# Kernel tuning notes

Hardware: AMD Instinct MI355X
Metric: run time of the kernel (lower is better)

## Reference

```python
import jax, jax.numpy as jnp
import numpy as np

NUM_CLASSES = 4
GAMMA = 2.0          # FocalLoss gamma
T_ALPHA, T_BETA = 0.3, 0.7
SMOOTH = 1e-5
W_DICE, W_CE, W_BOUND = 1.0, 1.0, 0.01
INF = 1e12


def _dt1d(f):
    # min-plus 1D squared distance transform along last axis (brute Felzenszwalb)
    n = f.shape[-1]
    i = jnp.arange(n, dtype=f.dtype)
    d2 = (i[:, None] - i[None, :]) ** 2          # [n, n]
    return jnp.min(f[..., None, :] + d2, axis=-1)


def _edt(seed):
    # Euclidean distance from every voxel to the nearest True voxel in `seed`
    f = jnp.where(seed, 0.0, INF).astype(jnp.float32)
    for ax in range(f.ndim):
        f = jnp.moveaxis(_dt1d(jnp.moveaxis(f, ax, -1)), -1, ax)
    return jnp.sqrt(f)


def _sdf(mask):
    # signed distance map, matching compute_edt_map (mask: bool [D,H,W])
    s = mask.sum()
    size = mask.size
    dist_out = _edt(mask)        # scipy distance(1-mask)
    dist_in = _edt(~mask)        # scipy distance(mask)
    sdf = dist_out - dist_in
    sdf = jnp.where(s == 0, 1.0, jnp.where(s == size, -1.0, sdf))
    return sdf


def setup_inputs() -> dict:
    key = jax.random.key(0)
    k1, k2 = jax.random.split(key)
    preds = jax.random.normal(k1, (4, NUM_CLASSES, 64, 64, 64), dtype=jnp.float32)
    targets = jax.random.randint(k2, (4, 64, 64, 64), 0, NUM_CLASSES).astype(jnp.int64)
    return {"preds": preds, "targets": targets}


def reference(preds, targets):
    B = preds.shape[0]
    sp_dims = (2, 3, 4)

    probs = jax.nn.softmax(preds, axis=1)                       # [B,C,D,H,W]
    onehot = (targets[:, None] == jnp.arange(NUM_CLASSES)[None, :, None, None, None]).astype(preds.dtype)

    # ---- Tversky ----
    TP = jnp.sum(probs * onehot, axis=sp_dims)
    FP = jnp.sum(probs * (1.0 - onehot), axis=sp_dims)
    FN = jnp.sum((1.0 - probs) * onehot, axis=sp_dims)
    tversky = (TP + SMOOTH) / (TP + T_ALPHA * FP + T_BETA * FN + SMOOTH)
    l_dice = 1.0 - tversky.mean()

    # ---- Focal ----
    logp = jax.nn.log_softmax(preds, axis=1)
    ce = -jnp.take_along_axis(logp, targets[:, None], axis=1)[:, 0]   # [B,D,H,W]
    pt = jnp.exp(-ce)
    l_main = jnp.mean((1.0 - pt) ** GAMMA * ce)

    # ---- Boundary ----
    masks = targets[:, None] == jnp.arange(1, NUM_CLASSES)[None, :, None, None, None]  # [B,3,D,H,W] bool
    flat = masks.reshape((-1,) + masks.shape[2:])
    sdfs = jax.lax.map(_sdf, flat).reshape(masks.shape)               # [B,3,D,H,W]
    nonempty = jnp.sum(masks, axis=sp_dims) > 0                       # [B,3]
    contrib = jnp.mean(sdfs * probs[:, 1:NUM_CLASSES], axis=sp_dims)  # [B,3]
    l_bound = jnp.sum(jnp.where(nonempty, contrib, 0.0)) / (B * (NUM_CLASSES - 1) + 1e-8)

    return W_DICE * l_dice + W_CE * l_main + W_BOUND * l_bound
```

## Files before the change

kernel.cpp:

```cpp
#include <hip/hip_runtime.h>
#include <math.h>

#define SPATIAL 262144
#define NVOX    1048576
#define NVOL    12
#define FAR_D2  50000
#define NPART   13

typedef unsigned short u16x2 __attribute__((ext_vector_type(2)));
union pku { unsigned int u; u16x2 v; };

__device__ __forceinline__ unsigned int pk_min(unsigned int a, unsigned int b) {
    pku x, y; x.u = a; y.u = b;
    x.v = __builtin_elementwise_min(x.v, y.v);
    return x.u;
}
__device__ __forceinline__ unsigned int pk_max(unsigned int a, unsigned int b) {
    pku x, y; x.u = a; y.u = b;
    x.v = __builtin_elementwise_max(x.v, y.v);
    return x.u;
}

__device__ __forceinline__ int row_d2i(unsigned long long m, int i) {
    if (m == 0ull) return FAR_D2;
    unsigned long long right = m >> i;
    unsigned long long left  = m << (63 - i);
    int dr = right ? __builtin_ctzll(right) : 1000;
    int dl = left  ? __builtin_clzll(left)  : 1000;
    int d = (dr < dl) ? dr : dl;
    return d * d;
}

#define MINPLUS_PK(LA, ACC, LANE, W)                                            \
    {                                                                           \
        const int base = (W) * 8;                                               \
        _Pragma("unroll")                                                       \
        for (int jj = 0; jj < 8; ++jj) {                                        \
            unsigned int wv = LA[(base + jj) * 64 + (LANE)];                    \
            _Pragma("unroll")                                                   \
            for (int k = 0; k < 8; ++k) {                                       \
                int d = k - jj;                                                 \
                unsigned int dd = (unsigned int)(d * d);                        \
                ACC[k] = pk_min(ACC[k], wv + (dd | (dd << 16)));                \
            }                                                                   \
        }                                                                       \
        const int el_max = base, er_max = 56 - base;                            \
        int t = 1;                                                              \
        while (true) {                                                          \
            unsigned int am = 0;                                                \
            _Pragma("unroll")                                                   \
            for (int k = 0; k < 8; ++k) am = pk_max(am, ACC[k]);                \
            _Pragma("unroll")                                                   \
            for (int off = 32; off > 0; off >>= 1)                              \
                am = pk_max(am, (unsigned int)__shfl_xor((int)am, off, 64));    \
            int amx = (int)(am & 0xFFFFu), amy = (int)(am >> 16);               \
            int mm = (amx > amy) ? amx : amy;                                   \
            int dmax = (int)sqrtf((float)mm) + 1;     \
            int Tl = (dmax < el_max) ? dmax : el_max;                           \
            int Tr = (dmax < er_max) ? dmax : er_max;                           \
            int T = (Tl > Tr) ? Tl : Tr;                                        \
            if (t > T) break;                                                   \
            int tend = (T < t + 7) ? T : (t + 7);                               \
            for (; t <= tend; ++t) {                                            \
                if (t <= Tl) {                                                  \
                    unsigned int wv = LA[(base - t) * 64 + (LANE)];             \
                    _Pragma("unroll")                                           \
                    for (int k = 0; k < 8; ++k) {                               \
                        int d = t + k;                                          \
                        unsigned int dd = (unsigned int)(d * d);                \
                        ACC[k] = pk_min(ACC[k], wv + (dd | (dd << 16)));        \
                    }                                                           \
                }                                                               \
                if (t <= Tr) {                                                  \
                    unsigned int wv = LA[(base + 7 + t) * 64 + (LANE)];         \
                    _Pragma("unroll")                                           \
                    for (int k = 0; k < 8; ++k) {                               \
                        int d = t + 7 - k;                                      \
                        unsigned int dd = (unsigned int)(d * d);                \
                        ACC[k] = pk_min(ACC[k], wv + (dd | (dd << 16)));        \
                    }                                                           \
                }                                                               \
            }                                                                   \
        }                                                                       \
    }

__global__ __launch_bounds__(512) void dtxy_kernel(
        const int* __restrict__ targets, unsigned int* __restrict__ dtp) {
    __shared__ unsigned int la[4096];
    int blk = blockIdx.x;
    int v = blk >> 6, z = blk & 63;
    int b = v / 3, cls = (v % 3) + 1;
    const int* tp = targets + b * SPATIAL + z * 4096;
    int t = threadIdx.x, lane = t & 63, w = t >> 6;

    #pragma unroll
    for (int k = 0; k < 8; ++k) {
        int y = w * 8 + k;
        int tv = tp[y * 64 + lane];
        unsigned long long m = __ballot(tv == cls);
        int do2 = row_d2i(m, lane);
        int di2 = row_d2i(~m, lane);
        la[y * 64 + lane] = (unsigned int)do2 | ((unsigned int)di2 << 16);
    }
    __syncthreads();

    unsigned int acc[8];
    #pragma unroll
    for (int k = 0; k < 8; ++k) acc[k] = 0xFFFFFFFFu;
    MINPLUS_PK(la, acc, lane, w)

    size_t vol = (size_t)v * SPATIAL;
    #pragma unroll
    for (int k = 0; k < 8; ++k) {
        int i = w * 8 + k;
        dtp[vol + (size_t)z * 4096 + (size_t)i * 64 + lane] = acc[k];
    }
}

__global__ __launch_bounds__(512) void dtz_fused_kernel(
        const unsigned int* __restrict__ dtp, const float* __restrict__ preds,
        const int* __restrict__ targets,
        float* __restrict__ bound, float* __restrict__ rpart) {
    __shared__ unsigned int la[4096];
    int blk = blockIdx.x;
    int v = blk >> 6, y = blk & 63;
    int b = v / 3, cls = (v % 3) + 1;
    size_t vol = (size_t)v * SPATIAL;
    int t = threadIdx.x, lane = t & 63, w = t >> 6;

    #pragma unroll
    for (int k = 0; k < 8; ++k) {
        int idx = k * 512 + t;
        int zz = idx >> 6, x = idx & 63;
        la[idx] = dtp[vol + (size_t)zz * 4096 + (size_t)y * 64 + x];
    }
    __syncthreads();

    unsigned int acc[8];
    #pragma unroll
    for (int k = 0; k < 8; ++k) acc[k] = 0xFFFFFFFFu;
    MINPLUS_PK(la, acc, lane, w)

    const bool doRed = (cls == 1);
    float loc[NPART];
    #pragma unroll
    for (int k = 0; k < NPART; ++k) loc[k] = 0.0f;

    float partial = 0.0f;
    const float* pbase = preds + (size_t)b * 4 * SPATIAL;
    const int* tbase = targets + b * SPATIAL;
    #pragma unroll
    for (int k = 0; k < 8; ++k) {
        int i = w * 8 + k;
        size_t sp = (size_t)i * 4096 + (size_t)y * 64 + lane;
        float dout = (float)(acc[k] & 0xFFFFu);
        float din  = (float)(acc[k] >> 16);
        float sv = sqrtf(dout) - sqrtf(din);
        float p0 = pbase[sp], p1 = pbase[SPATIAL + sp];
        float p2 = pbase[2 * SPATIAL + sp], p3 = pbase[3 * SPATIAL + sp];
        float m = fmaxf(fmaxf(p0, p1), fmaxf(p2, p3));
        float e0 = __expf(p0 - m), e1 = __expf(p1 - m);
        float e2 = __expf(p2 - m), e3 = __expf(p3 - m);
        float s = e0 + e1 + e2 + e3;
        float inv = __builtin_amdgcn_rcpf(s);
        float ec = (cls == 1) ? e1 : (cls == 2) ? e2 : e3;
        partial += sv * (ec * inv);
        if (doRed) {
            int tv = tbase[sp];
            float q0 = e0 * inv, q1 = e1 * inv, q2 = e2 * inv, q3 = e3 * inv;
            float pl = (tv == 0) ? p0 : (tv == 1) ? p1 : (tv == 2) ? p2 : p3;
            float ce = __logf(s) + (m - pl);
            float qt = (tv == 0) ? q0 : (tv == 1) ? q1 : (tv == 2) ? q2 : q3;
            float om = 1.0f - qt;
            loc[0] += q0; loc[1] += q1; loc[2] += q2; loc[3] += q3;
            if (tv == 0)      { loc[4] += q0; loc[8]  += 1.f; }
            else if (tv == 1) { loc[5] += q1; loc[9]  += 1.f; }
            else if (tv == 2) { loc[6] += q2; loc[10] += 1.f; }
            else              { loc[7] += q3; loc[11] += 1.f; }
            loc[12] += om * om * ce;
        }
    }

    #pragma unroll
    for (int off = 32; off > 0; off >>= 1)
        partial += __shfl_down(partial, off, 64);
    __shared__ float ws8[8];
    if (lane == 0) ws8[w] = partial;

    if (doRed) {
        __shared__ float sred[NPART][8];
        #pragma unroll
        for (int k = 0; k < NPART; ++k) {
            float vv = loc[k];
            #pragma unroll
            for (int off = 32; off > 0; off >>= 1)
                vv += __shfl_down(vv, off, 64);
            loc[k] = vv;
        }
        if (lane == 0) {
            #pragma unroll
            for (int k = 0; k < NPART; ++k) sred[k][w] = loc[k];
        }
        __syncthreads();
        if (t < NPART) {
            float tot = 0.0f;
            #pragma unroll
            for (int i = 0; i < 8; ++i) tot += sred[t][i];
            rpart[(b * NPART + t) * 64 + y] = tot;
        }
    } else {
        __syncthreads();
    }
    if (t == 0) {
        float tot = 0.0f;
        #pragma unroll
        for (int i = 0; i < 8; ++i) tot += ws8[i];
        bound[blk] = tot;
    }
}

__global__ __launch_bounds__(256) void final_kernel(
        const float* __restrict__ rpart, const float* __restrict__ bound,
        float* __restrict__ out) {
    __shared__ float rowsum[52];
    __shared__ float bsum[12];
    int tid = threadIdx.x, lane = tid & 63, w = tid >> 6;

    for (int r = w; r < 52; r += 4) {
        float v = rpart[r * 64 + lane];
        #pragma unroll
        for (int off = 32; off > 0; off >>= 1)
            v += __shfl_down(v, off, 64);
        if (lane == 0) rowsum[r] = v;
    }
    for (int r = w; r < 12; r += 4) {
        float v = bound[r * 64 + lane];
        #pragma unroll
        for (int off = 32; off > 0; off >>= 1)
            v += __shfl_down(v, off, 64);
        if (lane == 0) bsum[r] = v;
    }
    __syncthreads();
    if (tid != 0) return;

    float tsum = 0.0f;
    for (int b = 0; b < 4; ++b)
        for (int c = 0; c < 4; ++c) {
            float S  = rowsum[b * NPART + c];
            float TP = rowsum[b * NPART + 4 + c];
            float CN = rowsum[b * NPART + 8 + c];
            float FP = S - TP;
            float FN = CN - TP;
            tsum += (TP + 1e-5f) / (TP + 0.3f * FP + 0.7f * FN + 1e-5f);
        }
    float l_dice = 1.0f - tsum / 16.0f;
    float l_main = (rowsum[12] + rowsum[NPART + 12] +
                    rowsum[2 * NPART + 12] + rowsum[3 * NPART + 12]) / (float)NVOX;
    float bs = 0.0f;
    for (int v = 0; v < NVOL; ++v) {
        int b = v / 3, c = (v % 3) + 1;
        float CN = rowsum[b * NPART + 8 + c];
        float contrib;
        if (CN <= 0.0f) contrib = 0.0f;
        else if (CN >= (float)SPATIAL) contrib = -rowsum[b * NPART + c] / (float)SPATIAL;
        else contrib = bsum[v] / (float)SPATIAL;
        bs += contrib;
    }
    float l_bound = bs / (12.0f + 1e-8f);
    out[0] = l_dice + l_main + 0.01f * l_bound;
}

extern "C" void kernel_launch(void* const* d_in, const int* in_sizes, int n_in,
                              void* d_out, int out_size, void* d_ws, size_t ws_size,
                              hipStream_t stream) {
    const float* preds = (const float*)d_in[0];
    const int* targets = (const int*)d_in[1];
    float* out = (float*)d_out;
    float* ws = (float*)d_ws;
    float* rpart = ws;
    float* bound = ws + 4 * NPART * 64;
    unsigned int* dtp = (unsigned int*)(ws + 4 * NPART * 64 + NVOL * 64);

    hipLaunchKernelGGL(dtxy_kernel, dim3(NVOL * 64), dim3(512), 0, stream,
                       targets, dtp);
    hipLaunchKernelGGL(dtz_fused_kernel, dim3(NVOL * 64), dim3(512), 0, stream,
                       dtp, preds, targets, bound, rpart);
    hipLaunchKernelGGL(final_kernel, dim3(1), dim3(256), 0, stream,
                       rpart, bound, out);
}
```

Before: 104.0 us.

## Fold final reduction into dtz kernel via last-block atomic, vectorize dtp loads

Removes the separate final_kernel launch by having each dtz block atomically increment a counter (reset in dtxy_kernel) and letting the last block do the final reduction. The intent is to save one kernel launch plus its dependency gap. The dtp tile load into shared memory is also switched to 128-bit uint4 loads. The cost is a threadfence, an extra barrier and an atomic per block.

```diff
diff --git a/kernel.cpp b/kernel.cpp
--- a/kernel.cpp
+++ b/kernel.cpp
@@ -6,6 +6,7 @@
 #define NVOL    12
 #define FAR_D2  50000
 #define NPART   13
+#define NBLK    (NVOL * 64)
 
 typedef unsigned short u16x2 __attribute__((ext_vector_type(2)));
 union pku { unsigned int u; u16x2 v; };
@@ -85,9 +86,11 @@
     }
 
 __global__ __launch_bounds__(512) void dtxy_kernel(
-        const int* __restrict__ targets, unsigned int* __restrict__ dtp) {
+        const int* __restrict__ targets, unsigned int* __restrict__ dtp,
+        unsigned int* __restrict__ counter) {
     __shared__ unsigned int la[4096];
     int blk = blockIdx.x;
+    if (blk == 0 && threadIdx.x == 0) *counter = 0u;
     int v = blk >> 6, z = blk & 63;
     int b = v / 3, cls = (v % 3) + 1;
     const int* tp = targets + b * SPATIAL + z * 4096;
@@ -120,7 +123,8 @@
 __global__ __launch_bounds__(512) void dtz_fused_kernel(
         const unsigned int* __restrict__ dtp, const float* __restrict__ preds,
         const int* __restrict__ targets,
-        float* __restrict__ bound, float* __restrict__ rpart) {
+        float* __restrict__ bound, float* __restrict__ rpart,
+        unsigned int* __restrict__ counter, float* __restrict__ out) {
     __shared__ unsigned int la[4096];
     int blk = blockIdx.x;
     int v = blk >> 6, y = blk & 63;
@@ -129,10 +133,11 @@
     int t = threadIdx.x, lane = t & 63, w = t >> 6;
 
     #pragma unroll
-    for (int k = 0; k < 8; ++k) {
-        int idx = k * 512 + t;
-        int zz = idx >> 6, x = idx & 63;
-        la[idx] = dtp[vol + (size_t)zz * 4096 + (size_t)y * 64 + x];
+    for (int r = 0; r < 2; ++r) {
+        int zz = r * 32 + (t >> 4);
+        int x4 = (t & 15) << 2;
+        uint4 q = *(const uint4*)(dtp + vol + (size_t)zz * 4096 + ((size_t)y << 6) + x4);
+        *(uint4*)(&la[zz * 64 + x4]) = q;
     }
     __syncthreads();
 
@@ -217,38 +222,42 @@
         for (int i = 0; i < 8; ++i) tot += ws8[i];
         bound[blk] = tot;
     }
-}
-
-__global__ __launch_bounds__(256) void final_kernel(
-        const float* __restrict__ rpart, const float* __restrict__ bound,
-        float* __restrict__ out) {
+
+    __threadfence();
+    __syncthreads();
+    __shared__ unsigned int isLast;
+    if (t == 0) {
+        unsigned int old = atomicAdd(counter, 1u);
+        isLast = (old == (unsigned int)(NBLK - 1)) ? 1u : 0u;
+    }
+    __syncthreads();
+    if (!isLast) return;
+
     __shared__ float rowsum[52];
     __shared__ float bsum[12];
-    int tid = threadIdx.x, lane = tid & 63, w = tid >> 6;
-
-    for (int r = w; r < 52; r += 4) {
-        float v = rpart[r * 64 + lane];
+    for (int r = w; r < 52; r += 8) {
+        float vv = rpart[r * 64 + lane];
         #pragma unroll
         for (int off = 32; off > 0; off >>= 1)
-            v += __shfl_down(v, off, 64);
-        if (lane == 0) rowsum[r] = v;
-    }
-    for (int r = w; r < 12; r += 4) {
-        float v = bound[r * 64 + lane];
+            vv += __shfl_down(vv, off, 64);
+        if (lane == 0) rowsum[r] = vv;
+    }
+    for (int r = w; r < 12; r += 8) {
+        float vv = bound[r * 64 + lane];
         #pragma unroll
         for (int off = 32; off > 0; off >>= 1)
-            v += __shfl_down(v, off, 64);
-        if (lane == 0) bsum[r] = v;
-    }
-    __syncthreads();
-    if (tid != 0) return;
+            vv += __shfl_down(vv, off, 64);
+        if (lane == 0) bsum[r] = vv;
+    }
+    __syncthreads();
+    if (t != 0) return;
 
     float tsum = 0.0f;
-    for (int b = 0; b < 4; ++b)
+    for (int bb = 0; bb < 4; ++bb)
         for (int c = 0; c < 4; ++c) {
-            float S  = rowsum[b * NPART + c];
-            float TP = rowsum[b * NPART + 4 + c];
-            float CN = rowsum[b * NPART + 8 + c];
+            float S  = rowsum[bb * NPART + c];
+            float TP = rowsum[bb * NPART + 4 + c];
+            float CN = rowsum[bb * NPART + 8 + c];
             float FP = S - TP;
             float FN = CN - TP;
             tsum += (TP + 1e-5f) / (TP + 0.3f * FP + 0.7f * FN + 1e-5f);
@@ -257,13 +266,13 @@
     float l_main = (rowsum[12] + rowsum[NPART + 12] +
                     rowsum[2 * NPART + 12] + rowsum[3 * NPART + 12]) / (float)NVOX;
     float bs = 0.0f;
-    for (int v = 0; v < NVOL; ++v) {
-        int b = v / 3, c = (v % 3) + 1;
-        float CN = rowsum[b * NPART + 8 + c];
+    for (int vv = 0; vv < NVOL; ++vv) {
+        int bb = vv / 3, c = (vv % 3) + 1;
+        float CN = rowsum[bb * NPART + 8 + c];
         float contrib;
         if (CN <= 0.0f) contrib = 0.0f;
-        else if (CN >= (float)SPATIAL) contrib = -rowsum[b * NPART + c] / (float)SPATIAL;
-        else contrib = bsum[v] / (float)SPATIAL;
+        else if (CN >= (float)SPATIAL) contrib = -rowsum[bb * NPART + c] / (float)SPATIAL;
+        else contrib = bsum[vv] / (float)SPATIAL;
         bs += contrib;
     }
     float l_bound = bs / (12.0f + 1e-8f);
@@ -279,12 +288,11 @@
     float* ws = (float*)d_ws;
     float* rpart = ws;
     float* bound = ws + 4 * NPART * 64;
-    unsigned int* dtp = (unsigned int*)(ws + 4 * NPART * 64 + NVOL * 64);
-
-    hipLaunchKernelGGL(dtxy_kernel, dim3(NVOL * 64), dim3(512), 0, stream,
-                       targets, dtp);
-    hipLaunchKernelGGL(dtz_fused_kernel, dim3(NVOL * 64), dim3(512), 0, stream,
-                       dtp, preds, targets, bound, rpart);
-    hipLaunchKernelGGL(final_kernel, dim3(1), dim3(256), 0, stream,
-                       rpart, bound, out);
-}
+    unsigned int* counter = (unsigned int*)(ws + 4096);
+    unsigned int* dtp = (unsigned int*)(ws + 4112);
+
+    hipLaunchKernelGGL(dtxy_kernel, dim3(NBLK), dim3(512), 0, stream,
+                       targets, dtp, counter);
+    hipLaunchKernelGGL(dtz_fused_kernel, dim3(NBLK), dim3(512), 0, stream,
+                       dtp, preds, targets, bound, rpart, counter, out);
+}
```

New measurement: 199.6 us. 91.9% more time.

## Balance focal/Tversky reduction across class blocks and vectorize dtp tile load

Applied to the files above, without the earlier changes.

Before, only the class-1 blocks did the per-voxel focal/Tversky reduction, so they carried far more work than the class-2 and class-3 blocks. The reduction is now split across all three class volumes by z-range (0-22, 22-43, 43-64), and each block writes per-volume partials that the final kernel sums. The shared-memory staging of the distance tile now uses 128-bit loads instead of scalar loads. This adds more partial rows and a per-voxel range check, and every block now runs the 13-value reduction.

```diff
diff --git a/kernel.cpp b/kernel.cpp
--- a/kernel.cpp
+++ b/kernel.cpp
@@ -6,6 +6,7 @@
 #define NVOL    12
 #define FAR_D2  50000
 #define NPART   13
+#define NBLK    (NVOL * 64)
 
 typedef unsigned short u16x2 __attribute__((ext_vector_type(2)));
 union pku { unsigned int u; u16x2 v; };
@@ -129,10 +130,11 @@
     int t = threadIdx.x, lane = t & 63, w = t >> 6;
 
     #pragma unroll
-    for (int k = 0; k < 8; ++k) {
-        int idx = k * 512 + t;
-        int zz = idx >> 6, x = idx & 63;
-        la[idx] = dtp[vol + (size_t)zz * 4096 + (size_t)y * 64 + x];
+    for (int r = 0; r < 2; ++r) {
+        int zz = r * 32 + (t >> 4);
+        int x4 = (t & 15) << 2;
+        uint4 q = *(const uint4*)(dtp + vol + (size_t)zz * 4096 + ((size_t)y << 6) + x4);
+        *(uint4*)(&la[zz * 64 + x4]) = q;
     }
     __syncthreads();
 
@@ -141,7 +143,9 @@
     for (int k = 0; k < 8; ++k) acc[k] = 0xFFFFFFFFu;
     MINPLUS_PK(la, acc, lane, w)
 
-    const bool doRed = (cls == 1);
+    const int zlo = (cls == 1) ? 0 : (cls == 2) ? 22 : 43;
+    const int zhi = (cls == 1) ? 22 : (cls == 2) ? 43 : 64;
+
     float loc[NPART];
     #pragma unroll
     for (int k = 0; k < NPART; ++k) loc[k] = 0.0f;
@@ -165,7 +169,7 @@
         float inv = __builtin_amdgcn_rcpf(s);
         float ec = (cls == 1) ? e1 : (cls == 2) ? e2 : e3;
         partial += sv * (ec * inv);
-        if (doRed) {
+        if (i >= zlo && i < zhi) {
             int tv = tbase[sp];
             float q0 = e0 * inv, q1 = e1 * inv, q2 = e2 * inv, q3 = e3 * inv;
             float pl = (tv == 0) ? p0 : (tv == 1) ? p1 : (tv == 2) ? p2 : p3;
@@ -187,29 +191,25 @@
     __shared__ float ws8[8];
     if (lane == 0) ws8[w] = partial;
 
-    if (doRed) {
-        __shared__ float sred[NPART][8];
-        #pragma unroll
-        for (int k = 0; k < NPART; ++k) {
-            float vv = loc[k];
-            #pragma unroll
-            for (int off = 32; off > 0; off >>= 1)
-                vv += __shfl_down(vv, off, 64);
-            loc[k] = vv;
-        }
-        if (lane == 0) {
-            #pragma unroll
-            for (int k = 0; k < NPART; ++k) sred[k][w] = loc[k];
-        }
-        __syncthreads();
-        if (t < NPART) {
-            float tot = 0.0f;
-            #pragma unroll
-            for (int i = 0; i < 8; ++i) tot += sred[t][i];
-            rpart[(b * NPART + t) * 64 + y] = tot;
-        }
-    } else {
-        __syncthreads();
+    __shared__ float sred[NPART][8];
+    #pragma unroll
+    for (int k = 0; k < NPART; ++k) {
+        float vv = loc[k];
+        #pragma unroll
+        for (int off = 32; off > 0; off >>= 1)
+            vv += __shfl_down(vv, off, 64);
+        loc[k] = vv;
+    }
+    if (lane == 0) {
+        #pragma unroll
+        for (int k = 0; k < NPART; ++k) sred[k][w] = loc[k];
+    }
+    __syncthreads();
+    if (t < NPART) {
+        float tot = 0.0f;
+        #pragma unroll
+        for (int i = 0; i < 8; ++i) tot += sred[t][i];
+        rpart[(v * NPART + t) * 64 + y] = tot;
     }
     if (t == 0) {
         float tot = 0.0f;
@@ -222,18 +222,18 @@
 __global__ __launch_bounds__(256) void final_kernel(
         const float* __restrict__ rpart, const float* __restrict__ bound,
         float* __restrict__ out) {
-    __shared__ float rowsum[52];
-    __shared__ float bsum[12];
+    __shared__ float rowsum[NVOL * NPART];
+    __shared__ float bsum[NVOL];
     int tid = threadIdx.x, lane = tid & 63, w = tid >> 6;
 
-    for (int r = w; r < 52; r += 4) {
+    for (int r = w; r < NVOL * NPART; r += 4) {
         float v = rpart[r * 64 + lane];
         #pragma unroll
         for (int off = 32; off > 0; off >>= 1)
             v += __shfl_down(v, off, 64);
         if (lane == 0) rowsum[r] = v;
     }
-    for (int r = w; r < 12; r += 4) {
+    for (int r = w; r < NVOL; r += 4) {
         float v = bound[r * 64 + lane];
         #pragma unroll
         for (int off = 32; off > 0; off >>= 1)
@@ -244,25 +244,32 @@
     if (tid != 0) return;
 
     float tsum = 0.0f;
+    float Sb[4][4], CNb[4][4];
     for (int b = 0; b < 4; ++b)
         for (int c = 0; c < 4; ++c) {
-            float S  = rowsum[b * NPART + c];
-            float TP = rowsum[b * NPART + 4 + c];
-            float CN = rowsum[b * NPART + 8 + c];
+            float S = 0.f, TP = 0.f, CN = 0.f;
+            for (int vi = 0; vi < 3; ++vi) {
+                const float* rs = rowsum + (b * 3 + vi) * NPART;
+                S  += rs[c];
+                TP += rs[4 + c];
+                CN += rs[8 + c];
+            }
+            Sb[b][c] = S; CNb[b][c] = CN;
             float FP = S - TP;
             float FN = CN - TP;
             tsum += (TP + 1e-5f) / (TP + 0.3f * FP + 0.7f * FN + 1e-5f);
         }
     float l_dice = 1.0f - tsum / 16.0f;
-    float l_main = (rowsum[12] + rowsum[NPART + 12] +
-                    rowsum[2 * NPART + 12] + rowsum[3 * NPART + 12]) / (float)NVOX;
+    float fsum = 0.0f;
+    for (int v = 0; v < NVOL; ++v) fsum += rowsum[v * NPART + 12];
+    float l_main = fsum / (float)NVOX;
     float bs = 0.0f;
     for (int v = 0; v < NVOL; ++v) {
         int b = v / 3, c = (v % 3) + 1;
-        float CN = rowsum[b * NPART + 8 + c];
+        float CN = CNb[b][c];
         float contrib;
         if (CN <= 0.0f) contrib = 0.0f;
-        else if (CN >= (float)SPATIAL) contrib = -rowsum[b * NPART + c] / (float)SPATIAL;
+        else if (CN >= (float)SPATIAL) contrib = -Sb[b][c] / (float)SPATIAL;
         else contrib = bsum[v] / (float)SPATIAL;
         bs += contrib;
     }
@@ -278,12 +285,12 @@
     float* out = (float*)d_out;
     float* ws = (float*)d_ws;
     float* rpart = ws;
-    float* bound = ws + 4 * NPART * 64;
-    unsigned int* dtp = (unsigned int*)(ws + 4 * NPART * 64 + NVOL * 64);
-
-    hipLaunchKernelGGL(dtxy_kernel, dim3(NVOL * 64), dim3(512), 0, stream,
+    float* bound = ws + NVOL * NPART * 64;
+    unsigned int* dtp = (unsigned int*)(ws + 10752);
+
+    hipLaunchKernelGGL(dtxy_kernel, dim3(NBLK), dim3(512), 0, stream,
                        targets, dtp);
-    hipLaunchKernelGGL(dtz_fused_kernel, dim3(NVOL * 64), dim3(512), 0, stream,
+    hipLaunchKernelGGL(dtz_fused_kernel, dim3(NBLK), dim3(512), 0, stream,
                        dtp, preds, targets, bound, rpart);
     hipLaunchKernelGGL(final_kernel, dim3(1), dim3(256), 0, stream,
                        rpart, bound, out);
```

Result: slower. 116.3 us (+11.8%).
